# Kernel tuning notes

Hardware: AMD Instinct MI355X
Metric: run time of the kernel (lower is better)

The kernel has to match this reference:

```python
import jax, jax.numpy as jnp
import numpy as np

DIM = 768
H = 12
HD = 64  # head_dim = dim // num_heads
SCALE = HD ** (-0.5)
EPS = 1e-6


def setup_inputs() -> dict:
    key = jax.random.key(0)
    k1, k2, k3, k4, k5 = jax.random.split(key, 5)
    B, N = 8, 1024
    x = jax.random.normal(k1, (B, N, DIM), dtype=jnp.float32)
    policy = jax.random.uniform(k2, (B, N, 1), dtype=jnp.float32)
    # nn.Linear weights: [out_features, in_features]; qkv_bias=False, proj has bias
    qkv_w = jax.random.normal(k3, (3 * H * HD, DIM), dtype=jnp.float32) * (DIM ** -0.5)
    proj_w = jax.random.normal(k4, (DIM, H * HD), dtype=jnp.float32) * ((H * HD) ** -0.5)
    proj_b = jax.random.normal(k5, (DIM,), dtype=jnp.float32) * 0.01
    return {"x": x, "policy": policy, "qkv_w": qkv_w, "proj_w": proj_w, "proj_b": proj_b}


def _softmax_with_policy(attn, policy):
    # attn: [B,H,N,N], policy: [B,N,1]
    B, Hh, N, _ = attn.shape
    attn_policy = policy.reshape(B, 1, 1, N)
    eye = jnp.eye(N, dtype=attn_policy.dtype).reshape(1, 1, N, N)
    attn_policy = attn_policy + (1.0 - attn_policy) * eye
    max_att = jnp.max(attn, axis=-1, keepdims=True)
    a = jnp.exp((attn - max_att).astype(jnp.float32)) * attn_policy.astype(jnp.float32)
    a = (a + EPS / N) / (jnp.sum(a, axis=-1, keepdims=True) + EPS)
    return a.astype(max_att.dtype)


def reference(x, policy, qkv_w, proj_w, proj_b):
    B, N, C = x.shape
    qkv = (x @ qkv_w.T).reshape(B, N, 3, H, HD)
    qkv = jnp.transpose(qkv, (2, 0, 3, 1, 4))  # [3,B,H,N,HD]
    q, k, v = qkv[0], qkv[1], qkv[2]
    attn = jnp.einsum('bhnd,bhmd->bhnm', q * SCALE, k)  # [B,H,N,N]
    attn = _softmax_with_policy(attn, policy)
    out = jnp.einsum('bhnm,bhmd->bhnd', attn, v)  # [B,H,N,HD]
    out = jnp.transpose(out, (0, 2, 1, 3)).reshape(B, N, H * HD)
    return out @ proj_w.T + proj_b
```

## Files before the change

kernel.cpp:

```cpp
#include <hip/hip_runtime.h>

typedef __bf16 bf16x8 __attribute__((ext_vector_type(8)));
typedef float floatx4 __attribute__((ext_vector_type(4)));

#define EPSF 1e-6f

__device__ inline unsigned short f2bf(float f) {
  union { float f; unsigned u; } x; x.f = f;
  unsigned r = x.u + 0x7FFFu + ((x.u >> 16) & 1u);
  return (unsigned short)(r >> 16);
}
__device__ inline float bf2f(unsigned short u) {
  union { unsigned u; float f; } x; x.u = ((unsigned)u) << 16;
  return x.f;
}
__device__ inline unsigned pk2bf(float lo, float hi) {
  union { float f; unsigned u; } a, b; a.f = lo; b.f = hi;
  unsigned ua = a.u + 0x8000u, ub = b.u + 0x8000u;
  return (ub & 0xFFFF0000u) | (ua >> 16);
}

__device__ inline floatx4 mfma16(bf16x8 a, bf16x8 b, floatx4 c) {
  return __builtin_amdgcn_mfma_f32_16x16x32_bf16(a, b, c, 0, 0, 0);
}

__device__ inline void gll16(const unsigned short* g, unsigned short* l) {
  __builtin_amdgcn_global_load_lds((__attribute__((address_space(1))) void*)g,
                                   (__attribute__((address_space(3))) void*)l, 16, 0, 0);
}

__global__ __launch_bounds__(256) void cast_bf16_kernel(const float* __restrict__ in,
                                                        unsigned short* __restrict__ out,
                                                        int n, int n_scaled) {
  int i = (blockIdx.x * 256 + threadIdx.x) * 8;
  if (i >= n) return;
  const float s = (i < n_scaled) ? 0.18033688011112042f : 1.0f;
  float4 v0 = *(const float4*)(in + i);
  float4 v1 = *(const float4*)(in + i + 4);
  __align__(16) unsigned short o[8] = {
      f2bf(v0.x * s), f2bf(v0.y * s), f2bf(v0.z * s), f2bf(v0.w * s),
      f2bf(v1.x * s), f2bf(v1.y * s), f2bf(v1.z * s), f2bf(v1.w * s)};
  *(float4*)(out + i) = *(float4*)o;
}

__global__ __launch_bounds__(256) void policy_pack(const float* __restrict__ policy,
                                                   unsigned short* __restrict__ pbf) {
  int idx = blockIdx.x * 256 + threadIdx.x;
  int b = idx >> 10, g = idx & 1023;
  int chunk = g >> 5, w = g & 31;
  int c = (chunk << 5) + (w >> 1) + ((w & 1) << 4);
  pbf[idx] = f2bf(policy[b * 1024 + c]);
}

template <int EP, int BN>
__global__ __launch_bounds__(256, 3) void gemm_bt(const unsigned short* __restrict__ A,
                                                  const unsigned short* __restrict__ Bt,
                                                  void* __restrict__ Cout,
                                                  const float* __restrict__ bias,
                                                  int M, int N, int K) {
  constexpr int J = BN / 32;
  __shared__ __align__(16) unsigned short sA[128 * 64];
  __shared__ __align__(16) unsigned short sB[BN * 64];
  const int m0 = blockIdx.y * 128, n0 = blockIdx.x * BN;
  const int tid = threadIdx.x;
  const int lane = tid & 63, wave = tid >> 6;
  const int qd = lane >> 4, l15 = lane & 15;
  const int wr = (wave >> 1) * 64, wc = (wave & 1) * (BN / 2);
  const int srow = tid >> 3;
  const int scb = (tid & 7) ^ (srow & 7);
  const unsigned short* Ag = A + (long)(m0 + srow) * K + scb * 8;
  const unsigned short* Bg = Bt + (long)(n0 + srow) * K + scb * 8;
  const int x7 = l15 & 7;
  floatx4 acc[4][J] = {};
  for (int k0 = 0; k0 < K; k0 += 64) {
    __syncthreads();
#pragma unroll
    for (int p = 0; p < 4; p++) gll16(Ag + (long)(p * 32) * K + k0, sA + p * 2048 + wave * 512);
#pragma unroll
    for (int p = 0; p < J; p++) gll16(Bg + (long)(p * 32) * K + k0, sB + p * 2048 + wave * 512);
    __syncthreads();
#pragma unroll
    for (int s = 0; s < 2; s++) {
      const int cw = ((s * 4 + qd) ^ x7) * 8;
      bf16x8 af[4], bf[J];
#pragma unroll
      for (int i = 0; i < 4; i++) af[i] = *(const bf16x8*)&sA[(wr + i * 16 + l15) * 64 + cw];
#pragma unroll
      for (int j = 0; j < J; j++) bf[j] = *(const bf16x8*)&sB[(wc + j * 16 + l15) * 64 + cw];
#pragma unroll
      for (int i = 0; i < 4; i++)
#pragma unroll
        for (int j = 0; j < J; j++) acc[i][j] = mfma16(af[i], bf[j], acc[i][j]);
    }
  }
#pragma unroll
  for (int i = 0; i < 4; i++) {
#pragma unroll
    for (int j = 0; j < J; j++) {
      const int col = n0 + wc + j * 16 + l15;
#pragma unroll
      for (int r = 0; r < 4; r++) {
        const int row = m0 + wr + i * 16 + qd * 4 + r;
        if (EP == 0) {
          ((unsigned short*)Cout)[(long)row * N + col] = f2bf(acc[i][j][r]);
        } else {
          ((float*)Cout)[(long)row * N + col] = acc[i][j][r] + bias[col];
        }
      }
    }
  }
}

__global__ __launch_bounds__(256) void transpose_v(const unsigned short* __restrict__ qkv,
                                                   const float* __restrict__ policy,
                                                   unsigned short* __restrict__ vTp) {
  __shared__ unsigned short tile[64][72];
  __shared__ float sPol[64];
  const int bh = blockIdx.y;
  const int b = bh / 12, h = bh % 12;
  const int n0 = blockIdx.x * 64;
  const int t = threadIdx.x;
  if (t < 64) sPol[t] = policy[b * 1024 + n0 + t];
  {
    const int nr = t >> 2, dc = (t & 3) * 16;
    const unsigned short* src = qkv + (long)(b * 1024 + n0 + nr) * 2304 + 2 * 768 + h * 64 + dc;
    float4 v0 = *(const float4*)src;
    float4 v1 = *(const float4*)(src + 8);
    *(float4*)&tile[nr][dc] = v0;
    *(float4*)&tile[nr][dc + 8] = v1;
  }
  __syncthreads();
  {
    const int d = t >> 2, nc = (t & 3) * 16;
    __align__(16) unsigned short o[16];
#pragma unroll
    for (int jj = 0; jj < 16; jj++) {
      const int cc = nc + jj;
      const int w = cc & 31;
      const int cl = (cc & 32) + (w >> 1) + ((w & 1) << 4);
      o[jj] = f2bf(bf2f(tile[cl][d]) * sPol[cl]);
    }
    unsigned short* dst = vTp + (long)(bh * 64 + d) * 1024 + n0 + nc;
    *(float4*)dst = *(float4*)&o[0];
    *(float4*)(dst + 8) = *(float4*)&o[8];
  }
}

__global__ __launch_bounds__(256, 3) void attn_kernel(const unsigned short* __restrict__ qkv,
                                                      const unsigned short* __restrict__ vTp,
                                                      const unsigned short* __restrict__ pbf,
                                                      const float* __restrict__ policy,
                                                      unsigned short* __restrict__ aout) {
  __shared__ __align__(16) unsigned short sK[32 * 64];
  __shared__ __align__(16) unsigned short sV[64 * 32];
  __shared__ __align__(16) unsigned short sP[4][2][2][640];
  __shared__ __align__(16) unsigned short sPv[1024];
  __shared__ float sD[4][32];
  const int bid = blockIdx.x;
  const int bh = bid % 96, qt = bid / 96;
  const int b = bh / 12, h = bh % 12;
  const int tid = threadIdx.x;
  const int wave = tid >> 6, lane = tid & 63;
  const int qd = lane >> 4, l15 = lane & 15;
  const int q0 = qt * 128 + wave * 32;
  const unsigned short* qb = qkv + (long)(b * 1024 + q0 + l15) * 2304 + h * 64 + qd * 8;
  bf16x8 qf00 = *(const bf16x8*)qb;
  bf16x8 qf01 = *(const bf16x8*)(qb + 32);
  bf16x8 qf10 = *(const bf16x8*)(qb + (long)16 * 2304);
  bf16x8 qf11 = *(const bf16x8*)(qb + (long)16 * 2304 + 32);
  if (tid < 128) *(float4*)(sPv + tid * 8) = *(const float4*)(pbf + b * 1024 + tid * 8);
  const int krow = wave * 8 + (lane >> 3);
  const int kcb = (lane & 7) ^ (lane >> 3);
  const unsigned short* kgl = qkv + (long)(b * 1024 + krow) * 2304 + 768 + h * 64 + kcb * 8;
  const int vrow = tid >> 2;
  const int vcb = (tid & 3) ^ ((vrow ^ (vrow >> 2)) & 3);
  const unsigned short* vgl = vTp + (long)(bh * 64 + vrow) * 1024 + vcb * 8;
  const int x7 = l15 & 7;
  const int vsw = (qd ^ ((l15 ^ (l15 >> 2)) & 3)) * 8;
  floatx4 O0[4] = {}, O1[4] = {};
  floatx4 Dl0 = {}, Dl1 = {};
  for (int it = 0; it < 32; ++it) {
    const int c0 = it * 32;
    __syncthreads();
    gll16(kgl + (long)c0 * 2304, sK + wave * 512);
    gll16(vgl + c0, sV + wave * 512);
    __syncthreads();
    bf16x8 k00 = *(const bf16x8*)&sK[(0 * 16 + l15) * 64 + ((0 * 4 + qd) ^ x7) * 8];
    bf16x8 k01 = *(const bf16x8*)&sK[(0 * 16 + l15) * 64 + ((1 * 4 + qd) ^ x7) * 8];
    bf16x8 k10 = *(const bf16x8*)&sK[(1 * 16 + l15) * 64 + ((0 * 4 + qd) ^ x7) * 8];
    bf16x8 k11 = *(const bf16x8*)&sK[(1 * 16 + l15) * 64 + ((1 * 4 + qd) ^ x7) * 8];
    bf16x8 pv = *(const bf16x8*)&sPv[c0 + qd * 8];
    floatx4 z = {0.f, 0.f, 0.f, 0.f};
    floatx4 s00 = mfma16(qf01, k01, mfma16(qf00, k00, z));
    floatx4 s01 = mfma16(qf01, k11, mfma16(qf00, k10, z));
    floatx4 s10 = mfma16(qf11, k01, mfma16(qf10, k00, z));
    floatx4 s11 = mfma16(qf11, k11, mfma16(qf10, k10, z));
    unsigned short* w0 = &sP[wave][it & 1][0][0];
    unsigned short* w1 = &sP[wave][it & 1][1][0];
#pragma unroll
    for (int r = 0; r < 4; r++) {
      const int row = qd * 4 + r;
      ((unsigned*)w0)[row * 20 + l15] = pk2bf(exp2f(s00[r]), exp2f(s01[r]));
      ((unsigned*)w1)[row * 20 + l15] = pk2bf(exp2f(s10[r]), exp2f(s11[r]));
    }
    bf16x8 pf0 = *(const bf16x8*)&w0[l15 * 40 + qd * 8];
    bf16x8 pf1 = *(const bf16x8*)&w1[l15 * 40 + qd * 8];
    bf16x8 vf0 = *(const bf16x8*)&sV[(0 * 16 + l15) * 32 + vsw];
    bf16x8 vf1 = *(const bf16x8*)&sV[(1 * 16 + l15) * 32 + vsw];
    bf16x8 vf2 = *(const bf16x8*)&sV[(2 * 16 + l15) * 32 + vsw];
    bf16x8 vf3 = *(const bf16x8*)&sV[(3 * 16 + l15) * 32 + vsw];
    Dl0 = mfma16(pf0, pv, Dl0);
    Dl1 = mfma16(pf1, pv, Dl1);
    O0[0] = mfma16(pf0, vf0, O0[0]); O1[0] = mfma16(pf1, vf0, O1[0]);
    O0[1] = mfma16(pf0, vf1, O0[1]); O1[1] = mfma16(pf1, vf1, O1[1]);
    O0[2] = mfma16(pf0, vf2, O0[2]); O1[2] = mfma16(pf1, vf2, O1[2]);
    O0[3] = mfma16(pf0, vf3, O0[3]); O1[3] = mfma16(pf1, vf3, O1[3]);
  }
  {
    const unsigned short* kd = qkv + (long)(b * 1024 + q0 + l15) * 2304 + 768 + h * 64 + qd * 8;
    bf16x8 kd00 = *(const bf16x8*)kd;
    bf16x8 kd01 = *(const bf16x8*)(kd + 32);
    bf16x8 kd10 = *(const bf16x8*)(kd + (long)16 * 2304);
    bf16x8 kd11 = *(const bf16x8*)(kd + (long)16 * 2304 + 32);
    float part0 = 0.f, part1 = 0.f;
#pragma unroll
    for (int jj = 0; jj < 8; jj++) {
      part0 += (float)qf00[jj] * (float)kd00[jj] + (float)qf01[jj] * (float)kd01[jj];
      part1 += (float)qf10[jj] * (float)kd10[jj] + (float)qf11[jj] * (float)kd11[jj];
    }
    part0 += __shfl_xor(part0, 16); part0 += __shfl_xor(part0, 32);
    part1 += __shfl_xor(part1, 16); part1 += __shfl_xor(part1, 32);
    const float p0 = policy[b * 1024 + q0 + l15];
    const float p1 = policy[b * 1024 + q0 + 16 + l15];
    if (qd == 0) {
      sD[wave][l15] = exp2f(part0) * (1.0f - p0);
      sD[wave][16 + l15] = exp2f(part1) * (1.0f - p1);
    }
    __builtin_amdgcn_s_waitcnt(0);
    const unsigned short* vdiag = qkv + (long)(b * 1024 + q0) * 2304 + 1536 + h * 64 + l15;
#pragma unroll
    for (int r = 0; r < 4; r++) {
      const int row = qd * 4 + r;
      const float c0v = sD[wave][row], c1v = sD[wave][16 + row];
#pragma unroll
      for (int j = 0; j < 4; j++) {
        O0[j][r] += c0v * bf2f(vdiag[(long)row * 2304 + j * 16]);
        O1[j][r] += c1v * bf2f(vdiag[(long)(16 + row) * 2304 + j * 16]);
      }
      Dl0[r] += c0v;
      Dl1[r] += c1v;
    }
  }
  const long ob = (long)(b * 1024 + q0 + qd * 4) * 768 + h * 64 + l15;
#pragma unroll
  for (int r = 0; r < 4; r++) {
    const float li0 = 1.0f / (Dl0[r] + EPSF);
    const float li1 = 1.0f / (Dl1[r] + EPSF);
#pragma unroll
    for (int j = 0; j < 4; j++) {
      aout[ob + (long)r * 768 + j * 16] = f2bf(O0[j][r] * li0);
      aout[ob + (long)(16 * 768) + r * 768 + j * 16] = f2bf(O1[j][r] * li1);
    }
  }
}

extern "C" void kernel_launch(void* const* d_in, const int* in_sizes, int n_in,
                              void* d_out, int out_size, void* d_ws, size_t ws_size,
                              hipStream_t stream) {
  const float* x      = (const float*)d_in[0];
  const float* policy = (const float*)d_in[1];
  const float* qkv_w  = (const float*)d_in[2];
  const float* proj_w = (const float*)d_in[3];
  const float* proj_b = (const float*)d_in[4];
  float* out = (float*)d_out;

  char* ws = (char*)d_ws;
  unsigned short* xb    = (unsigned short*)(ws + 0);
  unsigned short* wqkv  = (unsigned short*)(ws + 12582912);
  unsigned short* wproj = (unsigned short*)(ws + 16121856);
  unsigned short* qkvb  = (unsigned short*)(ws + 17301504);
  unsigned short* vTp   = (unsigned short*)(ws + 55050240);
  unsigned short* aoutb = (unsigned short*)(ws + 67633152);
  unsigned short* pbf   = (unsigned short*)(ws + 80216064);

  cast_bf16_kernel<<<3072, 256, 0, stream>>>(x, xb, 6291456, 0);
  cast_bf16_kernel<<<864, 256, 0, stream>>>(qkv_w, wqkv, 1769472, 589824);
  cast_bf16_kernel<<<288, 256, 0, stream>>>(proj_w, wproj, 589824, 0);
  policy_pack<<<32, 256, 0, stream>>>(policy, pbf);
  gemm_bt<0, 128><<<dim3(18, 64), 256, 0, stream>>>(xb, wqkv, qkvb, nullptr, 8192, 2304, 768);
  transpose_v<<<dim3(16, 96), 256, 0, stream>>>(qkvb, policy, vTp);
  attn_kernel<<<dim3(768), 256, 0, stream>>>(qkvb, vTp, pbf, policy, aoutb);
  gemm_bt<1, 64><<<dim3(12, 64), 256, 0, stream>>>(aoutb, wproj, out, proj_b, 8192, 768, 768);
}
```

Baseline: 211.9 us.

## Double-buffer attention K/V tiles, pack QKV GEMM stores, fuse prep kernels

The attention loop now double-buffers K and V tiles in LDS. The next tile's global-to-LDS load is issued before computing on the current one, which removes one of the two barriers per iteration and hides load latency. The QKV GEMM epilogue now writes four bf16 values per store. This permutes columns within each 64-wide head block, and the permutation is undone by reordering the projection weight columns during the cast. The four cast and pack launches are merged into one prep kernel to cut launch overhead. The trade-off is more LDS use and a full waitcnt on every iteration.

Result: faster. 199.9 us (-5.6%).

```diff
diff --git a/kernel.cpp b/kernel.cpp
--- a/kernel.cpp
+++ b/kernel.cpp
@@ -29,27 +29,49 @@
                                    (__attribute__((address_space(3))) void*)l, 16, 0, 0);
 }
 
-__global__ __launch_bounds__(256) void cast_bf16_kernel(const float* __restrict__ in,
-                                                        unsigned short* __restrict__ out,
-                                                        int n, int n_scaled) {
-  int i = (blockIdx.x * 256 + threadIdx.x) * 8;
-  if (i >= n) return;
-  const float s = (i < n_scaled) ? 0.18033688011112042f : 1.0f;
-  float4 v0 = *(const float4*)(in + i);
-  float4 v1 = *(const float4*)(in + i + 4);
-  __align__(16) unsigned short o[8] = {
-      f2bf(v0.x * s), f2bf(v0.y * s), f2bf(v0.z * s), f2bf(v0.w * s),
-      f2bf(v1.x * s), f2bf(v1.y * s), f2bf(v1.z * s), f2bf(v1.w * s)};
-  *(float4*)(out + i) = *(float4*)o;
-}
-
-__global__ __launch_bounds__(256) void policy_pack(const float* __restrict__ policy,
+__global__ __launch_bounds__(256) void prep_kernel(const float* __restrict__ x,
+                                                   const float* __restrict__ qkv_w,
+                                                   const float* __restrict__ proj_w,
+                                                   const float* __restrict__ policy,
+                                                   unsigned short* __restrict__ xb,
+                                                   unsigned short* __restrict__ wqkv,
+                                                   unsigned short* __restrict__ wproj,
                                                    unsigned short* __restrict__ pbf) {
-  int idx = blockIdx.x * 256 + threadIdx.x;
-  int b = idx >> 10, g = idx & 1023;
-  int chunk = g >> 5, w = g & 31;
-  int c = (chunk << 5) + (w >> 1) + ((w & 1) << 4);
-  pbf[idx] = f2bf(policy[b * 1024 + c]);
+  const int bid = blockIdx.x, tid = threadIdx.x;
+  if (bid < 3072) {
+    const int i = bid * 2048 + tid * 8;
+    float4 v0 = *(const float4*)(x + i);
+    float4 v1 = *(const float4*)(x + i + 4);
+    __align__(16) unsigned short o[8] = {f2bf(v0.x), f2bf(v0.y), f2bf(v0.z), f2bf(v0.w),
+                                         f2bf(v1.x), f2bf(v1.y), f2bf(v1.z), f2bf(v1.w)};
+    *(float4*)(xb + i) = *(float4*)o;
+  } else if (bid < 3936) {
+    const int i = (bid - 3072) * 2048 + tid * 8;
+    const float s = (i < 589824) ? 0.18033688011112042f : 1.0f;
+    float4 v0 = *(const float4*)(qkv_w + i);
+    float4 v1 = *(const float4*)(qkv_w + i + 4);
+    __align__(16) unsigned short o[8] = {
+        f2bf(v0.x * s), f2bf(v0.y * s), f2bf(v0.z * s), f2bf(v0.w * s),
+        f2bf(v1.x * s), f2bf(v1.y * s), f2bf(v1.z * s), f2bf(v1.w * s)};
+    *(float4*)(wqkv + i) = *(float4*)o;
+  } else if (bid < 4224) {
+    const int i0 = (bid - 3936) * 2048 + tid * 8;
+    const int base = (i0 / 768) * 768 + ((i0 % 768) & ~63);
+    __align__(16) unsigned short o[8];
+#pragma unroll
+    for (int t = 0; t < 8; t++) {
+      const int cp = (i0 + t) & 63;
+      const int c = 16 * (cp & 3) + (cp >> 2);
+      o[t] = f2bf(proj_w[base + c]);
+    }
+    *(float4*)(wproj + i0) = *(float4*)o;
+  } else {
+    const int idx = (bid - 4224) * 256 + tid;
+    const int b = idx >> 10, g = idx & 1023;
+    const int chunk = g >> 5, w = g & 31;
+    const int c = (chunk << 5) + (w >> 1) + ((w & 1) << 4);
+    pbf[idx] = f2bf(policy[b * 1024 + c]);
+  }
 }
 
 template <int EP, int BN>
@@ -93,21 +115,29 @@
         for (int j = 0; j < J; j++) acc[i][j] = mfma16(af[i], bf[j], acc[i][j]);
     }
   }
-#pragma unroll
-  for (int i = 0; i < 4; i++) {
-#pragma unroll
-    for (int j = 0; j < J; j++) {
-      const int col = n0 + wc + j * 16 + l15;
+  if constexpr (EP == 0) {
+#pragma unroll
+    for (int i = 0; i < 4; i++)
 #pragma unroll
       for (int r = 0; r < 4; r++) {
         const int row = m0 + wr + i * 16 + qd * 4 + r;
-        if (EP == 0) {
-          ((unsigned short*)Cout)[(long)row * N + col] = f2bf(acc[i][j][r]);
-        } else {
+        __align__(8) unsigned short pk[4];
+#pragma unroll
+        for (int j = 0; j < 4; j++) pk[j] = f2bf(acc[i][j][r]);
+        *(uint2*)((unsigned short*)Cout + (long)row * N + n0 + wc + 4 * l15) = *(uint2*)pk;
+      }
+  } else {
+#pragma unroll
+    for (int i = 0; i < 4; i++)
+#pragma unroll
+      for (int j = 0; j < J; j++) {
+        const int col = n0 + wc + j * 16 + l15;
+#pragma unroll
+        for (int r = 0; r < 4; r++) {
+          const int row = m0 + wr + i * 16 + qd * 4 + r;
           ((float*)Cout)[(long)row * N + col] = acc[i][j][r] + bias[col];
         }
       }
-    }
   }
 }
 
@@ -151,8 +181,8 @@
                                                       const unsigned short* __restrict__ pbf,
                                                       const float* __restrict__ policy,
                                                       unsigned short* __restrict__ aout) {
-  __shared__ __align__(16) unsigned short sK[32 * 64];
-  __shared__ __align__(16) unsigned short sV[64 * 32];
+  __shared__ __align__(16) unsigned short sK[2][2048];
+  __shared__ __align__(16) unsigned short sV[2][2048];
   __shared__ __align__(16) unsigned short sP[4][2][2][640];
   __shared__ __align__(16) unsigned short sPv[1024];
   __shared__ float sD[4][32];
@@ -179,24 +209,29 @@
   const int vsw = (qd ^ ((l15 ^ (l15 >> 2)) & 3)) * 8;
   floatx4 O0[4] = {}, O1[4] = {};
   floatx4 Dl0 = {}, Dl1 = {};
+  gll16(kgl, &sK[0][wave * 512]);
+  gll16(vgl, &sV[0][wave * 512]);
+  __builtin_amdgcn_s_waitcnt(0);
+  __syncthreads();
   for (int it = 0; it < 32; ++it) {
+    const int buf = it & 1;
+    if (it < 31) {
+      gll16(kgl + (long)(32 * (it + 1)) * 2304, &sK[buf ^ 1][wave * 512]);
+      gll16(vgl + 32 * (it + 1), &sV[buf ^ 1][wave * 512]);
+    }
     const int c0 = it * 32;
-    __syncthreads();
-    gll16(kgl + (long)c0 * 2304, sK + wave * 512);
-    gll16(vgl + c0, sV + wave * 512);
-    __syncthreads();
-    bf16x8 k00 = *(const bf16x8*)&sK[(0 * 16 + l15) * 64 + ((0 * 4 + qd) ^ x7) * 8];
-    bf16x8 k01 = *(const bf16x8*)&sK[(0 * 16 + l15) * 64 + ((1 * 4 + qd) ^ x7) * 8];
-    bf16x8 k10 = *(const bf16x8*)&sK[(1 * 16 + l15) * 64 + ((0 * 4 + qd) ^ x7) * 8];
-    bf16x8 k11 = *(const bf16x8*)&sK[(1 * 16 + l15) * 64 + ((1 * 4 + qd) ^ x7) * 8];
+    bf16x8 k00 = *(const bf16x8*)&sK[buf][(0 * 16 + l15) * 64 + ((0 * 4 + qd) ^ x7) * 8];
+    bf16x8 k01 = *(const bf16x8*)&sK[buf][(0 * 16 + l15) * 64 + ((1 * 4 + qd) ^ x7) * 8];
+    bf16x8 k10 = *(const bf16x8*)&sK[buf][(1 * 16 + l15) * 64 + ((0 * 4 + qd) ^ x7) * 8];
+    bf16x8 k11 = *(const bf16x8*)&sK[buf][(1 * 16 + l15) * 64 + ((1 * 4 + qd) ^ x7) * 8];
     bf16x8 pv = *(const bf16x8*)&sPv[c0 + qd * 8];
     floatx4 z = {0.f, 0.f, 0.f, 0.f};
     floatx4 s00 = mfma16(qf01, k01, mfma16(qf00, k00, z));
     floatx4 s01 = mfma16(qf01, k11, mfma16(qf00, k10, z));
     floatx4 s10 = mfma16(qf11, k01, mfma16(qf10, k00, z));
     floatx4 s11 = mfma16(qf11, k11, mfma16(qf10, k10, z));
-    unsigned short* w0 = &sP[wave][it & 1][0][0];
-    unsigned short* w1 = &sP[wave][it & 1][1][0];
+    unsigned short* w0 = &sP[wave][buf][0][0];
+    unsigned short* w1 = &sP[wave][buf][1][0];
 #pragma unroll
     for (int r = 0; r < 4; r++) {
       const int row = qd * 4 + r;
@@ -205,16 +240,18 @@
     }
     bf16x8 pf0 = *(const bf16x8*)&w0[l15 * 40 + qd * 8];
     bf16x8 pf1 = *(const bf16x8*)&w1[l15 * 40 + qd * 8];
-    bf16x8 vf0 = *(const bf16x8*)&sV[(0 * 16 + l15) * 32 + vsw];
-    bf16x8 vf1 = *(const bf16x8*)&sV[(1 * 16 + l15) * 32 + vsw];
-    bf16x8 vf2 = *(const bf16x8*)&sV[(2 * 16 + l15) * 32 + vsw];
-    bf16x8 vf3 = *(const bf16x8*)&sV[(3 * 16 + l15) * 32 + vsw];
+    bf16x8 vf0 = *(const bf16x8*)&sV[buf][(0 * 16 + l15) * 32 + vsw];
+    bf16x8 vf1 = *(const bf16x8*)&sV[buf][(1 * 16 + l15) * 32 + vsw];
+    bf16x8 vf2 = *(const bf16x8*)&sV[buf][(2 * 16 + l15) * 32 + vsw];
+    bf16x8 vf3 = *(const bf16x8*)&sV[buf][(3 * 16 + l15) * 32 + vsw];
     Dl0 = mfma16(pf0, pv, Dl0);
     Dl1 = mfma16(pf1, pv, Dl1);
     O0[0] = mfma16(pf0, vf0, O0[0]); O1[0] = mfma16(pf1, vf0, O1[0]);
     O0[1] = mfma16(pf0, vf1, O0[1]); O1[1] = mfma16(pf1, vf1, O1[1]);
     O0[2] = mfma16(pf0, vf2, O0[2]); O1[2] = mfma16(pf1, vf2, O1[2]);
     O0[3] = mfma16(pf0, vf3, O0[3]); O1[3] = mfma16(pf1, vf3, O1[3]);
+    __builtin_amdgcn_s_waitcnt(0);
+    __syncthreads();
   }
   {
     const unsigned short* kd = qkv + (long)(b * 1024 + q0 + l15) * 2304 + 768 + h * 64 + qd * 8;
@@ -283,10 +320,7 @@
   unsigned short* aoutb = (unsigned short*)(ws + 67633152);
   unsigned short* pbf   = (unsigned short*)(ws + 80216064);
 
-  cast_bf16_kernel<<<3072, 256, 0, stream>>>(x, xb, 6291456, 0);
-  cast_bf16_kernel<<<864, 256, 0, stream>>>(qkv_w, wqkv, 1769472, 589824);
-  cast_bf16_kernel<<<288, 256, 0, stream>>>(proj_w, wproj, 589824, 0);
-  policy_pack<<<32, 256, 0, stream>>>(policy, pbf);
+  prep_kernel<<<4256, 256, 0, stream>>>(x, qkv_w, proj_w, policy, xb, wqkv, wproj, pbf);
   gemm_bt<0, 128><<<dim3(18, 64), 256, 0, stream>>>(xb, wqkv, qkvb, nullptr, 8192, 2304, 768);
   transpose_v<<<dim3(16, 96), 256, 0, stream>>>(qkvb, policy, vTp);
   attn_kernel<<<dim3(768), 256, 0, stream>>>(qkvb, vTp, pbf, policy, aoutb);
```
